# Kernel tuning notes

Measured on AMD Instinct MI355X. Metric: run time of the kernel, lower is better.

Reference implementation:

```python
import jax, jax.numpy as jnp
import numpy as np

B, N, DIM = 2, 2048, 1024
H, DH = 16, 64
DIM_INNER = H * DH
EPS = float(jnp.finfo(jnp.float32).eps)  # torch nn.RMSNorm default eps = finfo.eps
THETA = 10000.0


def setup_inputs() -> dict:
    key = jax.random.key(0)
    ks = jax.random.split(key, 6)
    s = 0.02
    tokens = jax.random.normal(ks[0], (B, N, DIM), dtype=jnp.float32)
    w_norm = jnp.ones((DIM,), jnp.float32)                      # prenorm RMSNorm weight
    w_q = jax.random.normal(ks[1], (DIM, DIM_INNER), jnp.float32) * s
    w_k = jax.random.normal(ks[2], (DIM, 3 * DIM_INNER), jnp.float32) * s
    w_v = jax.random.normal(ks[3], (DIM, 3 * DIM_INNER), jnp.float32) * s
    w_key_norms = jnp.ones((3, DH), jnp.float32)                # 3 key RMSNorms
    w_nested_knorm = jnp.ones((DH,), jnp.float32)
    w_out = jax.random.normal(ks[4], (DIM_INNER, DIM), jnp.float32) * s
    return {"tokens": tokens, "w_norm": w_norm, "w_q": w_q, "w_k": w_k,
            "w_v": w_v, "w_key_norms": w_key_norms,
            "w_nested_knorm": w_nested_knorm, "w_out": w_out}


def rmsnorm(x, w):
    var = jnp.mean(jnp.square(x), axis=-1, keepdims=True)
    return x * jax.lax.rsqrt(var + EPS) * w


def rope(x):
    # interleaved (GPT-J style) rotary, as in rotary_embedding_torch defaults
    n, d = x.shape[-2], x.shape[-1]
    inv_freq = 1.0 / (THETA ** (jnp.arange(0, d, 2, dtype=jnp.float32) / d))
    freqs = jnp.arange(n, dtype=jnp.float32)[:, None] * inv_freq   # (n, d/2)
    cos = jnp.repeat(jnp.cos(freqs), 2, axis=-1)                   # (n, d)
    sin = jnp.repeat(jnp.sin(freqs), 2, axis=-1)
    x1, x2 = x[..., ::2], x[..., 1::2]
    x_rot = jnp.stack((-x2, x1), axis=-1).reshape(x.shape)         # rotate_half
    return x * cos + x_rot * sin


def attend(q, k, v):
    # rotate_queries_with_cached_keys with equal lengths -> plain rotary on both
    q = rope(q)
    k = rope(k)
    d = q.shape[-1]
    scores = jnp.einsum('bhqd,bhkd->bhqk', q, k) / jnp.sqrt(jnp.float32(d))
    n = scores.shape[-1]
    causal = jnp.tril(jnp.ones((n, n), dtype=bool))
    scores = jnp.where(causal, scores, -jnp.inf)
    attn = jax.nn.softmax(scores, axis=-1)
    return jnp.einsum('bhqk,bhkd->bhqd', attn, v)


def reference(tokens, w_norm, w_q, w_k, w_v, w_key_norms, w_nested_knorm, w_out):
    b, n = tokens.shape[:2]
    x = rmsnorm(tokens, w_norm)                                    # prenorm
    q = (x @ w_q).reshape(b, n, H, DH).transpose(0, 2, 1, 3)       # (b,h,n,d)
    # chunk(3, dim=-1) then split heads -> (3,b,h,n,d)
    ks = (x @ w_k).reshape(b, n, 3, H, DH).transpose(2, 0, 3, 1, 4)
    vs = (x @ w_v).reshape(b, n, 3, H, DH).transpose(2, 0, 3, 1, 4)
    ks = rmsnorm(ks, w_key_norms[:, None, None, None, :])          # per-branch key norm
    # three parallel causal attentions sharing the same queries
    nq, nk, nv = jax.vmap(attend, in_axes=(None, 0, 0))(q, ks, vs)
    nk = rmsnorm(nk, w_nested_knorm)
    out = attend(nq, nk, nv)                                       # nested attention
    out = out.transpose(0, 2, 1, 3).reshape(b, n, DIM_INNER)       # merge heads
    return out @ w_out
```

## Files before the change

kernel.cpp:

```cpp
#include <hip/hip_runtime.h>
#include <hip/hip_bf16.h>
#include <stdint.h>

typedef unsigned short u16;
typedef __attribute__((ext_vector_type(8))) short short8;
typedef __attribute__((ext_vector_type(4))) float float4v;
typedef __attribute__((ext_vector_type(4))) unsigned int uint4v;

#define B_    2
#define N_    2048
#define DIM_  1024
#define H_    16
#define DH_   64
#define DI_   1024
#define EPS_  1.1920928955078125e-07f
#define LOG2_THETA 13.287712379549449f
#define SCL_  0.18033688011112042f

__device__ __forceinline__ float bf2f(u16 u) {
    union { unsigned int i; float f; } v; v.i = ((unsigned int)u) << 16; return v.f;
}
__device__ __forceinline__ u16 f2bf(float f) {
    union { float f; unsigned int i; } v; v.f = f;
    unsigned int r = v.i + 0x7fff + ((v.i >> 16) & 1);
    return (u16)(r >> 16);
}
__device__ __forceinline__ unsigned int cvtpk(float a, float b) {
    unsigned int r;
    asm("v_cvt_pk_bf16_f32 %0, %1, %2" : "=v"(r) : "v"(a), "v"(b));
    return r;
}
__device__ __forceinline__ int perm32(int n) {
    return (n & ~31) + (((n >> 2) & 3) * 8) + (((n >> 4) & 1) * 4) + (n & 3);
}

__global__ __launch_bounds__(256) void k_pre(
    const float* __restrict__ w_q, const float* __restrict__ w_k,
    const float* __restrict__ w_v, u16* __restrict__ dstW,
    const float* __restrict__ tok, const float* __restrict__ w_norm,
    u16* __restrict__ xn) {
    int bx = blockIdx.x;
    int t = threadIdx.x;
    __shared__ float tile[32][33];
    __shared__ float red[4];
    if (bx < 7168) {
        int c0 = (bx % 224) * 32, k0 = (bx / 224) * 32;
        const float* src; int sN, sc0;
        if (c0 < 1024)      { src = w_q; sN = 1024; sc0 = c0; }
        else if (c0 < 4096) { src = w_k; sN = 3072; sc0 = c0 - 1024; }
        else                { src = w_v; sN = 3072; sc0 = c0 - 4096; }
        int tx = t & 31, ty = t >> 5;
#pragma unroll
        for (int i = 0; i < 4; ++i)
            tile[ty + 8 * i][tx] = src[(size_t)(k0 + ty + 8 * i) * sN + sc0 + tx];
        __syncthreads();
#pragma unroll
        for (int i = 0; i < 4; ++i)
            dstW[(size_t)(c0 + ty + 8 * i) * 1024 + k0 + tx] = f2bf(tile[tx][ty + 8 * i]);
    } else {
        int row = bx - 7168;
        const float* tr = tok + (size_t)row * DIM_ + t * 4;
        float4v v = *(const float4v*)tr;
        float ss = v[0] * v[0] + v[1] * v[1] + v[2] * v[2] + v[3] * v[3];
#pragma unroll
        for (int o = 32; o; o >>= 1) ss += __shfl_xor(ss, o, 64);
        if ((t & 63) == 0) red[t >> 6] = ss;
        __syncthreads();
        ss = red[0] + red[1] + red[2] + red[3];
        float rs = rsqrtf(ss * (1.0f / DIM_) + EPS_);
        const float* wp = w_norm + t * 4;
        uint2 pk;
        pk.x = cvtpk(v[0] * rs * wp[0], v[1] * rs * wp[1]);
        pk.y = cvtpk(v[2] * rs * wp[2], v[3] * rs * wp[3]);
        *(uint2*)(xn + (size_t)row * DIM_ + t * 4) = pk;
    }
}

__global__ __launch_bounds__(256) void k_transpose(
    const float* __restrict__ src, u16* __restrict__ dst, int K, int N) {
    __shared__ float tile[32][33];
    int n0 = blockIdx.x * 32, k0 = blockIdx.y * 32;
    int tx = threadIdx.x, ty = threadIdx.y;
#pragma unroll
    for (int i = 0; i < 4; ++i)
        tile[ty + 8 * i][tx] = src[(size_t)(k0 + ty + 8 * i) * N + n0 + tx];
    __syncthreads();
#pragma unroll
    for (int i = 0; i < 4; ++i)
        dst[(size_t)(n0 + ty + 8 * i) * K + k0 + tx] = f2bf(tile[tx][ty + 8 * i]);
}

__global__ __launch_bounds__(256) void k_post1(
    u16* __restrict__ QKVB, u16* __restrict__ Vt, const float* __restrict__ w) {
    int bx = blockIdx.x;
    int t = threadIdx.x;
    __shared__ u16 tile[64][72];
    if (bx < 3072) {
        int y = bx >> 5;
        int s = y >> 5;
        int b = (y >> 4) & 1;
        int h = y & 15;
        int n0 = (bx & 31) * 64;
#pragma unroll
        for (int i = 0; i < 2; ++i) {
            int idx = i * 256 + t;
            int row = idx >> 3, c = idx & 7;
            uint4v v = *(const uint4v*)(QKVB + ((size_t)(b * N_) + n0 + row) * 7168
                                            + 4096 + s * 1024 + h * 64 + c * 8);
            *(uint4v*)&tile[row][c * 8] = v;
        }
        __syncthreads();
        u16* out = Vt + (size_t)y * 64 * N_;
#pragma unroll
        for (int i = 0; i < 2; ++i) {
            int idx = i * 256 + t;
            int dh = idx >> 3, og = idx & 7;
            u16 vals[8];
#pragma unroll
            for (int j = 0; j < 8; ++j) {
                int m = og * 8 + j;
                int nn = (m & 32) + (m & 3) + ((m >> 3) & 3) * 4 + ((m >> 2) & 1) * 16;
                vals[j] = tile[nn][dh];
            }
            *(uint4v*)(out + (size_t)dh * N_ + n0 + og * 8) = *(const uint4v*)vals;
        }
    } else {
        int wid = (bx - 3072) * 4 + (t >> 6);
        int lane = t & 63;
        int r8 = lane >> 3, e8 = lane & 7;
        int hg = wid & 1;
        int s = (wid >> 1) % 3;
        int row = wid / 6;
        int n = row & (N_ - 1);
        int h = hg * 8 + r8;
        u16* p = QKVB + (size_t)row * 7168 + 1024 + s * 1024 + h * 64 + e8 * 8;
        uint4v v = *(const uint4v*)p;
        float x[8];
#pragma unroll
        for (int j = 0; j < 8; ++j) x[j] = bf2f(((const u16*)&v)[j]);
        float ss = 0.f;
#pragma unroll
        for (int j = 0; j < 8; ++j) ss += x[j] * x[j];
        ss += __shfl_xor(ss, 1, 64);
        ss += __shfl_xor(ss, 2, 64);
        ss += __shfl_xor(ss, 4, 64);
        float rs = rsqrtf(ss * (1.0f / 64.0f) + EPS_);
        const float* ws = w + s * 64 + e8 * 8;
        uint4v pk;
#pragma unroll
        for (int tp = 0; tp < 4; ++tp) {
            int d0 = e8 * 8 + 2 * tp;
            float xn0 = x[2 * tp] * rs * ws[2 * tp];
            float xn1 = x[2 * tp + 1] * rs * ws[2 * tp + 1];
            float inv = exp2f(-(float)d0 * (LOG2_THETA / 64.0f));
            float fr = (float)n * inv;
            float sv, cv;
            __sincosf(fr, &sv, &cv);
            pk[tp] = cvtpk(xn0 * cv - xn1 * sv, xn1 * cv + xn0 * sv);
        }
        *(uint4v*)p = pk;
    }
}

template <bool OUT_F32>
__global__ __launch_bounds__(256) void k_gemm_bt(
    const u16* __restrict__ A, const u16* __restrict__ Bt, void* __restrict__ Cv,
    int K, int Ncols) {
    __shared__ u16 As[2][128 * 32];
    __shared__ u16 Bs[2][128 * 32];
    int m0 = blockIdx.x * 128, n0 = blockIdx.y * 128;
    int t = threadIdx.x;
    int w = t >> 6, lane = t & 63, ln = lane & 15, quad = lane >> 4;
    int wm = w & 1, wn = w >> 1;
    float4v acc[4][4] = {};
    const u16* Ag = A + (size_t)m0 * K;
    const u16* Bg = Bt + (size_t)n0 * K;

    auto stage = [&](int k0, int buf) {
#pragma unroll
        for (int i = 0; i < 2; ++i) {
            int idx = i * 256 + t;
            int row = idx >> 2, kb = idx & 3;
            int csrc = (kb ^ ((row >> 1) & 3)) * 8;
            const u16* ga = Ag + (size_t)row * K + k0 + csrc;
            const u16* gb = Bg + (size_t)row * K + k0 + csrc;
            __builtin_amdgcn_global_load_lds(
                (const __attribute__((address_space(1))) void*)ga,
                (__attribute__((address_space(3))) void*)(As[buf] + idx * 8), 16, 0, 0);
            __builtin_amdgcn_global_load_lds(
                (const __attribute__((address_space(1))) void*)gb,
                (__attribute__((address_space(3))) void*)(Bs[buf] + idx * 8), 16, 0, 0);
        }
    };

    int nk = K >> 5;
    stage(0, 0);
    int rchunk = (quad ^ ((ln >> 1) & 3)) * 8;

    for (int kt = 0; kt < nk; ++kt) {
        asm volatile("s_waitcnt vmcnt(0)" ::: "memory");
        __syncthreads();
        if (kt + 1 < nk) stage((kt + 1) << 5, (kt + 1) & 1);
        int buf = kt & 1;
        short8 af[4], bfr[4];
#pragma unroll
        for (int mt = 0; mt < 4; ++mt)
            af[mt] = *(const short8*)(As[buf] + (wm * 64 + mt * 16 + ln) * 32 + rchunk);
#pragma unroll
        for (int nt = 0; nt < 4; ++nt)
            bfr[nt] = *(const short8*)(Bs[buf] + (wn * 64 + nt * 16 + ln) * 32 + rchunk);
#pragma unroll
        for (int mt = 0; mt < 4; ++mt)
#pragma unroll
            for (int nt = 0; nt < 4; ++nt)
                acc[mt][nt] = __builtin_amdgcn_mfma_f32_16x16x32_bf16(
                    af[mt], bfr[nt], acc[mt][nt], 0, 0, 0);
    }
#pragma unroll
    for (int mt = 0; mt < 4; ++mt)
#pragma unroll
        for (int nt = 0; nt < 4; ++nt)
#pragma unroll
            for (int r = 0; r < 4; ++r) {
                int row = m0 + wm * 64 + mt * 16 + quad * 4 + r;
                int col = n0 + wn * 64 + nt * 16 + ln;
                if (OUT_F32)
                    ((float*)Cv)[(size_t)row * Ncols + col] = acc[mt][nt][r];
                else
                    ((u16*)Cv)[(size_t)row * Ncols + col] = f2bf(acc[mt][nt][r]);
            }
}

__global__ __launch_bounds__(256, 2) void k_flash(
    const u16* __restrict__ Q, int q_stride,
    const u16* __restrict__ K, const u16* __restrict__ Vt,
    u16* __restrict__ O, u16* __restrict__ Ot,
    int kv_stride, int set_off, size_t o_set_stride,
    const float* __restrict__ wnk) {
    int bh = blockIdx.x;
    int qt = gridDim.y - 1 - blockIdx.y;
    int s = blockIdx.z;
    int b = bh >> 4, h = bh & 15;
    int t = threadIdx.x;
    int w = t >> 6, lane = t & 63, ln = lane & 15, quad = lane >> 4;
    int lnx = ln & 7;
    int q0 = qt * 128;
    int qw = q0 + w * 32;

    const u16* Qb  = Q + ((size_t)b * N_) * q_stride + h * 64;
    const u16* Kb  = K + ((size_t)b * N_) * kv_stride + (size_t)s * set_off + h * 64;
    const u16* Vtb = Vt + (size_t)((s * B_ + b) * H_ + h) * (64 * (size_t)N_);

    __shared__ u16 Ks[2][2][64][64];
    __shared__ u16 Vs[2][2][64][64];

    short8 ones;
#pragma unroll
    for (int j = 0; j < 8; ++j) ((u16*)&ones)[j] = 0x3F80;

    short8 qf[2][2];
    float mrow[2];
    float4v accO[2][4] = {};
    float4v accL[2] = {};
#pragma unroll
    for (int g = 0; g < 2; ++g) {
        int qg = qw + g * 16;
        int tokn = qg + ln;
        short8 raw[2];
#pragma unroll
        for (int f = 0; f < 2; ++f)
            raw[f] = *(const short8*)(Qb + (size_t)tokn * q_stride + f * 32 + quad * 8);
        float qn = 0.f;
#pragma unroll
        for (int f = 0; f < 2; ++f)
#pragma unroll
            for (int j = 0; j < 8; ++j) {
                float v = bf2f(((const u16*)&raw[f])[j]);
                qn += v * v;
            }
        qn += __shfl_xor(qn, 16, 64);
        qn += __shfl_xor(qn, 32, 64);
        mrow[g] = sqrtf(qn) * (8.0f * SCL_) * 1.03f + 1e-6f;
#pragma unroll
        for (int f = 0; f < 2; ++f) {
            u16 out8[8];
            int dbase = f * 32 + quad * 8;
#pragma unroll
            for (int tp = 0; tp < 4; ++tp) {
                int d = dbase + 2 * tp;
                float inv = exp2f((float)d * (-LOG2_THETA / 64.0f));
                float fr = (float)tokn * inv;
                float sv, cv;
                __sincosf(fr, &sv, &cv);
                float x0 = bf2f(((const u16*)&raw[f])[2 * tp]);
                float x1 = bf2f(((const u16*)&raw[f])[2 * tp + 1]);
                out8[2 * tp]     = f2bf((x0 * cv - x1 * sv) * SCL_);
                out8[2 * tp + 1] = f2bf((x1 * cv + x0 * sv) * SCL_);
            }
            qf[g][f] = *(const short8*)out8;
        }
    }

    int ntb = 2 * qt + 2;
    int nwin = ntb >> 1;

    auto stage = [&](int win, int buf) {
#pragma unroll
        for (int sub = 0; sub < 2; ++sub) {
            int k0 = (win * 2 + sub) * 64;
#pragma unroll
            for (int i = 0; i < 2; ++i) {
                int idx = i * 256 + t;
                int row = idx >> 3, c = idx & 7;
                int csrc = ((c ^ (row & 7)) * 8);
                const u16* ga = Kb + (size_t)(k0 + row) * kv_stride + csrc;
                __builtin_amdgcn_global_load_lds(
                    (const __attribute__((address_space(1))) void*)ga,
                    (__attribute__((address_space(3))) void*)&Ks[buf][sub][row][c * 8], 16, 0, 0);
                const u16* gv = Vtb + (size_t)row * N_ + k0 + csrc;
                __builtin_amdgcn_global_load_lds(
                    (const __attribute__((address_space(1))) void*)gv,
                    (__attribute__((address_space(3))) void*)&Vs[buf][sub][row][c * 8], 16, 0, 0);
            }
        }
    };

    auto compute = [&](int buf, int sub, int k0) {
        short8 kf[4][2];
#pragma unroll
        for (int kt = 0; kt < 4; ++kt) {
            const u16* krow = &Ks[buf][sub][kt * 16 + ln][0];
            kf[kt][0] = *(const short8*)(krow + ((quad ^ lnx) * 8));
            kf[kt][1] = *(const short8*)(krow + (((4 + quad) ^ lnx) * 8));
        }
        short8 pb[2][2];
#pragma unroll
        for (int g = 0; g < 2; ++g) {
            int qg = qw + g * 16;
            float4v st[4];
#pragma unroll
            for (int kt = 0; kt < 4; ++kt) {
                float4v sa = {-mrow[g], -mrow[g], -mrow[g], -mrow[g]};
                sa = __builtin_amdgcn_mfma_f32_16x16x32_bf16(kf[kt][0], qf[g][0], sa, 0, 0, 0);
                sa = __builtin_amdgcn_mfma_f32_16x16x32_bf16(kf[kt][1], qf[g][1], sa, 0, 0, 0);
                st[kt] = sa;
            }
            if (k0 + 63 <= qg) {
#pragma unroll
                for (int c = 0; c < 2; ++c) {
                    uint4v pk;
#pragma unroll
                    for (int kt2 = 0; kt2 < 2; ++kt2) {
                        pk[kt2 * 2 + 0] = cvtpk(exp2f(st[c * 2 + kt2][0]),
                                                exp2f(st[c * 2 + kt2][1]));
                        pk[kt2 * 2 + 1] = cvtpk(exp2f(st[c * 2 + kt2][2]),
                                                exp2f(st[c * 2 + kt2][3]));
                    }
                    pb[g][c] = *(short8*)&pk;
                }
            } else {
                int qr = qg + ln;
#pragma unroll
                for (int c = 0; c < 2; ++c) {
                    uint4v pk;
#pragma unroll
                    for (int kt2 = 0; kt2 < 2; ++kt2) {
                        int kt = c * 2 + kt2;
                        float e[4];
#pragma unroll
                        for (int r = 0; r < 4; ++r) {
                            int kg = k0 + kt * 16 + quad * 4 + r;
                            float arg = (kg <= qr) ? st[kt][r] : -1e30f;
                            e[r] = exp2f(arg);
                        }
                        pk[kt2 * 2 + 0] = cvtpk(e[0], e[1]);
                        pk[kt2 * 2 + 1] = cvtpk(e[2], e[3]);
                    }
                    pb[g][c] = *(short8*)&pk;
                }
            }
        }
#pragma unroll
        for (int dc = 0; dc < 4; ++dc) {
            const u16* vrow = &Vs[buf][sub][dc * 16 + ln][0];
            short8 vf0 = *(const short8*)(vrow + ((quad ^ lnx) * 8));
            short8 vf1 = *(const short8*)(vrow + (((4 + quad) ^ lnx) * 8));
#pragma unroll
            for (int g = 0; g < 2; ++g) {
                accO[g][dc] = __builtin_amdgcn_mfma_f32_16x16x32_bf16(vf0, pb[g][0], accO[g][dc], 0, 0, 0);
                accO[g][dc] = __builtin_amdgcn_mfma_f32_16x16x32_bf16(vf1, pb[g][1], accO[g][dc], 0, 0, 0);
            }
        }
#pragma unroll
        for (int g = 0; g < 2; ++g) {
            accL[g] = __builtin_amdgcn_mfma_f32_16x16x32_bf16(ones, pb[g][0], accL[g], 0, 0, 0);
            accL[g] = __builtin_amdgcn_mfma_f32_16x16x32_bf16(ones, pb[g][1], accL[g], 0, 0, 0);
        }
    };

    stage(0, 0);

    for (int wv = 0; wv < nwin; ++wv) {
        asm volatile("s_waitcnt vmcnt(0)" ::: "memory");
        __syncthreads();
        if (wv + 1 < nwin) stage(wv + 1, (wv + 1) & 1);
        int buf = wv & 1;
        int k0 = wv * 128;
        if (k0 > qw + 31) continue;
        compute(buf, 0, k0);
        if (k0 + 64 <= qw + 31)
            compute(buf, 1, k0 + 64);
    }

#pragma unroll
    for (int g = 0; g < 2; ++g) {
        float rinv = 1.0f / accL[g][0];
        int qg = qw + g * 16;
        int qr = qg + ln;
        if (s == 2) {
            u16* Otb = Ot + (size_t)(b * H_ + h) * (64 * (size_t)N_);
            int pos = perm32(qr & (N_ - 1)) + (qr & ~(N_ - 1));
#pragma unroll
            for (int dc = 0; dc < 4; ++dc)
#pragma unroll
                for (int r = 0; r < 4; ++r)
                    Otb[(size_t)(dc * 16 + quad * 4 + r) * N_ + pos] =
                        f2bf(accO[g][dc][r] * rinv);
        } else if (wnk && s == 1) {
            u16* Ob = O + o_set_stride + ((size_t)b * N_) * DI_ + h * 64;
            float o[4][4];
            float ss = 0.f;
#pragma unroll
            for (int dc = 0; dc < 4; ++dc)
#pragma unroll
                for (int r = 0; r < 4; ++r) {
                    float x = accO[g][dc][r] * rinv;
                    o[dc][r] = x;
                    ss += x * x;
                }
            ss += __shfl_xor(ss, 16, 64);
            ss += __shfl_xor(ss, 32, 64);
            float rs2 = rsqrtf(ss * (1.0f / 64.0f) + EPS_);
#pragma unroll
            for (int dc = 0; dc < 4; ++dc) {
                uint2 pk;
#pragma unroll
                for (int rp = 0; rp < 2; ++rp) {
                    int d0 = dc * 16 + quad * 4 + 2 * rp;
                    float x0 = o[dc][2 * rp]     * rs2 * wnk[d0];
                    float x1 = o[dc][2 * rp + 1] * rs2 * wnk[d0 + 1];
                    float inv = exp2f(-(float)d0 * (LOG2_THETA / 64.0f));
                    float fr = (float)qr * inv;
                    float sv, cv;
                    __sincosf(fr, &sv, &cv);
                    unsigned int u = cvtpk(x0 * cv - x1 * sv, x1 * cv + x0 * sv);
                    if (rp == 0) pk.x = u; else pk.y = u;
                }
                *(uint2*)(Ob + (size_t)qr * DI_ + dc * 16 + quad * 4) = pk;
            }
        } else {
            u16* Ob = O + (size_t)s * o_set_stride + ((size_t)b * N_) * DI_ + h * 64;
#pragma unroll
            for (int dc = 0; dc < 4; ++dc) {
                uint2 pk;
                pk.x = cvtpk(accO[g][dc][0] * rinv, accO[g][dc][1] * rinv);
                pk.y = cvtpk(accO[g][dc][2] * rinv, accO[g][dc][3] * rinv);
                *(uint2*)(Ob + (size_t)qr * DI_ + dc * 16 + quad * 4) = pk;
            }
        }
    }
}

extern "C" void kernel_launch(void* const* d_in, const int* in_sizes, int n_in,
                              void* d_out, int out_size, void* d_ws, size_t ws_size,
                              hipStream_t stream) {
    const float* tok     = (const float*)d_in[0];
    const float* w_norm  = (const float*)d_in[1];
    const float* w_q     = (const float*)d_in[2];
    const float* w_k     = (const float*)d_in[3];
    const float* w_v     = (const float*)d_in[4];
    const float* w_keyn  = (const float*)d_in[5];
    const float* w_nestk = (const float*)d_in[6];
    const float* w_o     = (const float*)d_in[7];

    char* ws = (char*)d_ws;
    const size_t MB = 1024 * 1024;
    u16* QKVB  = (u16*)(ws + 0 * MB);
    u16* VtB   = (u16*)(ws + 56 * MB);
    u16* NQKV  = (u16*)(ws + 80 * MB);
    u16* WQKVT = (u16*)(ws + 80 * MB);
    u16* NVt   = (u16*)(ws + 96 * MB);
    u16* XN    = (u16*)(ws + 96 * MB);
    u16* OUT2  = (u16*)(ws + 104 * MB);
    u16* WOT   = (u16*)(ws + 80 * MB);

    const size_t SET = (size_t)B_ * N_ * DI_;

    k_pre<<<7168 + 4096, 256, 0, stream>>>(w_q, w_k, w_v, WQKVT, tok, w_norm, XN);

    k_gemm_bt<false><<<dim3(32, 56), 256, 0, stream>>>(XN, WQKVT, QKVB, 1024, 7168);

    k_post1<<<3072 + 6144, 256, 0, stream>>>(QKVB, VtB, w_keyn);

    k_flash<<<dim3(B_ * H_, N_ / 128, 3), 256, 0, stream>>>(
        QKVB, 7168, QKVB + 1024, VtB, NQKV, NVt, 7168, 1024, SET, w_nestk);

    k_flash<<<dim3(B_ * H_, N_ / 128, 1), 256, 0, stream>>>(
        NQKV, 1024, NQKV + SET, NVt, OUT2, NVt , 1024, 0, 0, nullptr);

    k_transpose<<<dim3(32, 32), dim3(32, 8), 0, stream>>>(w_o, WOT, 1024, 1024);
    k_gemm_bt<true><<<dim3(32, 8), 256, 0, stream>>>(OUT2, WOT, (float*)d_out, 1024, 1024);
}
```

Before: 367.1 us.

## Remap GEMM blocks across XCDs and template flash KV window size

The GEMM launch becomes a 1D grid whose block index is remapped so that consecutive tiles land on the same XCD (blockIdx & 7 chunking), which should improve L2 locality on the multi-die MI355X. The flash kernel is templated on the number of 64-key sub-tiles per staged window. The first attention pass uses one sub-tile, which halves LDS and raises the launch-bounds occupancy hint to 3, while the nested pass keeps two. A smaller window means more barriers per key range in exchange for higher occupancy.

After: 363.0 us. About the same (-1.1%).

```diff
diff --git a/kernel.cpp b/kernel.cpp
--- a/kernel.cpp
+++ b/kernel.cpp
@@ -166,9 +166,12 @@
 __global__ __launch_bounds__(256) void k_gemm_bt(
     const u16* __restrict__ A, const u16* __restrict__ Bt, void* __restrict__ Cv,
     int K, int Ncols) {
+    int nwg = gridDim.x;
+    int chunk = nwg >> 3;
+    int wg = (blockIdx.x & 7) * chunk + (blockIdx.x >> 3);
+    int m0 = (wg & 31) * 128, n0 = (wg >> 5) * 128;
     __shared__ u16 As[2][128 * 32];
     __shared__ u16 Bs[2][128 * 32];
-    int m0 = blockIdx.x * 128, n0 = blockIdx.y * 128;
     int t = threadIdx.x;
     int w = t >> 6, lane = t & 63, ln = lane & 15, quad = lane >> 4;
     int wm = w & 1, wn = w >> 1;
@@ -231,7 +234,8 @@
             }
 }
 
-__global__ __launch_bounds__(256, 2) void k_flash(
+template <int WIN>
+__global__ __launch_bounds__(256, WIN == 1 ? 3 : 2) void k_flash(
     const u16* __restrict__ Q, int q_stride,
     const u16* __restrict__ K, const u16* __restrict__ Vt,
     u16* __restrict__ O, u16* __restrict__ Ot,
@@ -251,8 +255,8 @@
     const u16* Kb  = K + ((size_t)b * N_) * kv_stride + (size_t)s * set_off + h * 64;
     const u16* Vtb = Vt + (size_t)((s * B_ + b) * H_ + h) * (64 * (size_t)N_);
 
-    __shared__ u16 Ks[2][2][64][64];
-    __shared__ u16 Vs[2][2][64][64];
+    __shared__ u16 Ks[2][WIN][64][64];
+    __shared__ u16 Vs[2][WIN][64][64];
 
     short8 ones;
 #pragma unroll
@@ -302,12 +306,12 @@
     }
 
     int ntb = 2 * qt + 2;
-    int nwin = ntb >> 1;
+    int nwin = ntb / WIN;
 
     auto stage = [&](int win, int buf) {
 #pragma unroll
-        for (int sub = 0; sub < 2; ++sub) {
-            int k0 = (win * 2 + sub) * 64;
+        for (int sub = 0; sub < WIN; ++sub) {
+            int k0 = (win * WIN + sub) * 64;
 #pragma unroll
             for (int i = 0; i < 2; ++i) {
                 int idx = i * 256 + t;
@@ -405,10 +409,10 @@
         __syncthreads();
         if (wv + 1 < nwin) stage(wv + 1, (wv + 1) & 1);
         int buf = wv & 1;
-        int k0 = wv * 128;
+        int k0 = wv * (WIN * 64);
         if (k0 > qw + 31) continue;
         compute(buf, 0, k0);
-        if (k0 + 64 <= qw + 31)
+        if (WIN == 2 && k0 + 64 <= qw + 31)
             compute(buf, 1, k0 + 64);
     }
 
@@ -498,16 +502,16 @@
 
     k_pre<<<7168 + 4096, 256, 0, stream>>>(w_q, w_k, w_v, WQKVT, tok, w_norm, XN);
 
-    k_gemm_bt<false><<<dim3(32, 56), 256, 0, stream>>>(XN, WQKVT, QKVB, 1024, 7168);
+    k_gemm_bt<false><<<1792, 256, 0, stream>>>(XN, WQKVT, QKVB, 1024, 7168);
 
     k_post1<<<3072 + 6144, 256, 0, stream>>>(QKVB, VtB, w_keyn);
 
-    k_flash<<<dim3(B_ * H_, N_ / 128, 3), 256, 0, stream>>>(
+    k_flash<1><<<dim3(B_ * H_, N_ / 128, 3), 256, 0, stream>>>(
         QKVB, 7168, QKVB + 1024, VtB, NQKV, NVt, 7168, 1024, SET, w_nestk);
 
-    k_flash<<<dim3(B_ * H_, N_ / 128, 1), 256, 0, stream>>>(
+    k_flash<2><<<dim3(B_ * H_, N_ / 128, 1), 256, 0, stream>>>(
         NQKV, 1024, NQKV + SET, NVt, OUT2, NVt , 1024, 0, 0, nullptr);
 
     k_transpose<<<dim3(32, 32), dim3(32, 8), 0, stream>>>(w_o, WOT, 1024, 1024);
-    k_gemm_bt<true><<<dim3(32, 8), 256, 0, stream>>>(OUT2, WOT, (float*)d_out, 1024, 1024);
-}
+    k_gemm_bt<true><<<256, 256, 0, stream>>>(OUT2, WOT, (float*)d_out, 1024, 1024);
+}
```
